# Optimization experiments

Hardware: AMD Instinct MI355X
Metric: run time of the kernel (lower is better)

Reference implementation:

```python
import jax, jax.numpy as jnp
import numpy as np

T_STEPS, N_GRID = 730, 8000
NEARZERO = 1e-5
# parameter bounds, order: tt ddf alpha beta stor retip fscn scx flz stot cgw resmax k1 k2 k3 k4 k5 k6
_BOUNDS = [(-3,5),(0,20),(0,1),(0,1),(0,5),(0,50),(0,1),(0,1),(0.005,0.995),(1,2000),(0,20),(1,300),(0,1),(1,5),(0,1),(0,1),(0,1),(0,1)]
_LO = jnp.array([b[0] for b in _BOUNDS], dtype=jnp.float32)
_HI = jnp.array([b[1] for b in _BOUNDS], dtype=jnp.float32)


def setup_inputs() -> dict:
    key = jax.random.key(0)
    kx, kp = jax.random.split(key)
    x = jax.random.uniform(kx, (T_STEPS, N_GRID, 3), dtype=jnp.float32)
    # scale forcings to physical ranges: prcp in [0,10) mm/d, tmean in [-2,6) C, pet in [0,5) mm/d
    x = x * jnp.array([10.0, 8.0, 5.0], dtype=jnp.float32) + jnp.array([0.0, -2.0, 0.0], dtype=jnp.float32)
    parameters = jax.random.normal(kp, (T_STEPS, N_GRID, 18), dtype=jnp.float32)
    return {"x": x, "parameters": parameters}


def _prms_forward(x, parameters):
    # static params: sigmoid of NN output at static_idx = warm_up - 1 = -1, scaled to bounds
    p = jax.nn.sigmoid(parameters[-1, :, :18])            # [N, 18]
    p = _LO + p * (_HI - _LO)
    p = p[:, :, None]                                      # [N, 18, 1]  (nmul = 1)
    (tt, ddf, alpha, beta, stor, retip, fscn, scx, flz, stot,
     cgw, resmax, k1, k2, k3, k4, k5, k6) = [p[:, i] for i in range(18)]
    scn = fscn * scx
    remx = (1.0 - flz) * stot
    smax = flz * stot

    Pm = x[:, :, 0:1]    # precipitation [T, N, 1]
    Tm = x[:, :, 1:2]    # mean temperature
    PETm = x[:, :, 2:3]  # potential ET

    n_grid = x.shape[1]
    s0 = jnp.full((n_grid, 1), 0.001, dtype=jnp.float32)
    init = (s0, s0, s0, s0, s0, s0, s0)  # snow, XIN, RSTOR, RECHR, SMAV, RES, GW

    def step(state, inp):
        snow, xin, rstor, rechr, smav, res, gw = state
        PRECIP, temp, Ep = inp
        # snow partition and melt (delta_t = 1)
        is_snow = (temp <= tt).astype(jnp.float32)
        flux_ps = PRECIP * is_snow
        flux_pr = PRECIP * (1.0 - is_snow)
        snow = snow + flux_ps
        flux_m = jnp.maximum(ddf * (temp - tt), 0.0)
        flux_m = jnp.minimum(flux_m, snow)
        snow = jnp.maximum(snow - flux_m, NEARZERO)
        # interception
        flux_pim = flux_pr * (1.0 - beta)
        flux_psm = flux_pr * beta
        flux_pby = flux_psm * (1.0 - alpha)
        flux_pin = flux_psm * alpha
        xin = xin + flux_pin
        flux_ptf = jnp.maximum(xin - stor, 0.0)
        xin = jnp.maximum(xin - flux_ptf, NEARZERO)
        flux_ein = jnp.minimum(Ep * beta, xin)
        xin = jnp.maximum(xin - flux_ein, NEARZERO)
        # impervious reservoir
        flux_mim = flux_m * (1.0 - beta)
        flux_msm = flux_m * beta
        rstor = rstor + flux_mim + flux_pim
        flux_sas = jnp.maximum(rstor - retip, 0.0)
        rstor = jnp.maximum(rstor - flux_sas, NEARZERO)
        flux_eim = jnp.minimum((1.0 - beta) * Ep, rstor)
        rstor = jnp.maximum(rstor - flux_eim, NEARZERO)
        # surface runoff / infiltration to recharge zone
        sro_lin = jnp.clip(scn + (scx - scn) * (rechr / remx), 0.0, 1.0)
        inflow = flux_msm + flux_ptf + flux_pby
        flux_sro = sro_lin * inflow
        flux_inf = inflow - flux_sro
        rechr = rechr + flux_inf
        flux_pc = jnp.maximum(rechr - remx, 0.0)
        rechr = rechr - flux_pc
        evap_max_a = jnp.maximum(rechr / remx * (Ep - flux_ein - flux_eim), 0.0)
        flux_ea = jnp.minimum(evap_max_a, rechr)
        rechr = jnp.maximum(rechr - flux_ea, NEARZERO)
        # lower soil moisture zone
        smav = smav + flux_pc
        flux_excs = jnp.maximum(smav - smax, 0.0)
        smav = smav - flux_excs
        transp = jnp.where(rechr < (Ep - flux_ein - flux_eim),
                           jnp.maximum(smav / smax * (Ep - flux_ein - flux_eim - flux_ea), 0.0),
                           jnp.zeros_like(smav))
        transp = jnp.minimum(transp, smav)
        smav = jnp.maximum(smav - transp, NEARZERO)
        # seepage and subsurface reservoir
        flux_sep = jnp.minimum(cgw, flux_excs)
        flux_qres = jnp.maximum(flux_excs - flux_sep, 0.0)
        res = res + flux_qres
        flux_gad = k1 * (res / resmax) ** k2
        flux_gad = jnp.minimum(flux_gad, res)
        res = jnp.maximum(res - flux_gad, NEARZERO)
        flux_ras = k3 * res + k4 * res * res
        flux_ras = jnp.minimum(flux_ras, res)
        res = jnp.maximum(res - flux_ras, NEARZERO)
        # groundwater
        gw = gw + flux_gad + flux_sep
        flux_bas = k5 * gw
        gw = jnp.maximum(gw - flux_bas, NEARZERO)
        flux_snk = k6 * gw
        gw = jnp.maximum(gw - flux_snk, NEARZERO)
        q = flux_sas + flux_sro + flux_bas + flux_ras
        return (snow, xin, rstor, rechr, smav, res, gw), q

    _, Q = jax.lax.scan(step, init, (Pm, Tm, PETm))
    return Q  # [T, N, 1]


def reference(x, parameters):
    return _prms_forward(x, parameters)
```

## Files before the change

### kernel.cpp

```cpp
#include <hip/hip_runtime.h>
#include <math.h>

#define T_STEPS 730
#define N_GRID  8000
#define NEARZERO 1e-5f

__constant__ float c_lo[18] = {-3.f, 0.f, 0.f, 0.f, 0.f, 0.f, 0.f, 0.f, 0.005f, 1.f,    0.f, 1.f,   0.f, 1.f, 0.f, 0.f, 0.f, 0.f};
__constant__ float c_hi[18] = { 5.f, 20.f, 1.f, 1.f, 5.f, 50.f, 1.f, 1.f, 0.995f, 2000.f, 20.f, 300.f, 1.f, 5.f, 1.f, 1.f, 1.f, 1.f};

#define EXP2F(v) __builtin_amdgcn_exp2f(v)
#define LOG2F(v) __builtin_amdgcn_logf(v)

constexpr int CH  = 10;
constexpr int NCH = T_STEPS / CH;

__global__ __launch_bounds__(256, 1) void prms_kernel(
    const float* __restrict__ x,
    const float* __restrict__ params,
    float* __restrict__ out)
{
    const int lane = threadIdx.x & 63;
    const int wv   = threadIdx.x >> 6;
    const int i    = blockIdx.x * 64 + lane;

    __shared__ float4 c0a[2][CH][64];
    __shared__ float4 c0b[2][CH][64];
    __shared__ float4 c1 [2][CH][64];
    __shared__ float2 c2 [2][CH][64];

    const float* pp = params + ((size_t)(T_STEPS - 1) * N_GRID + (size_t)i) * 18;
    float pr[18];
#pragma unroll
    for (int j = 0; j < 18; ++j) {
        float s = 1.0f / (1.0f + expf(-pp[j]));
        pr[j] = c_lo[j] + s * (c_hi[j] - c_lo[j]);
    }
    const float tt = pr[0],  ddf = pr[1], alpha = pr[2], beta = pr[3];
    const float stor = pr[4], retip = pr[5], fscn = pr[6], scx = pr[7];
    const float flz = pr[8],  stot = pr[9], cgw = pr[10], resmax = pr[11];
    const float k1 = pr[12],  k2 = pr[13], k3 = pr[14], k4 = pr[15];
    const float k5 = pr[16],  k6 = pr[17];

    const float ombeta   = 1.0f - beta;
    const float omalpha  = 1.0f - alpha;
    const float scn      = fscn * scx;
    const float remx     = (1.0f - flz) * stot;
    const float smax     = flz * stot;
    const float inv_remx = 1.0f / remx;
    const float inv_smax = 1.0f / smax;
    const float omscn    = 1.0f - scn;
    const float omk3     = 1.0f - k3;
    const float omk56    = (1.0f - k5) * (1.0f - k6);
    const float dscn     = (scx - scn) * inv_remx;
    const float pow_c2   = fmaf(k2, LOG2F(1.0f / resmax), LOG2F(k1));

    if (wv == 0) {
        float snow = 0.001f;
        float3 buf[CH];
#pragma unroll
        for (int u = 0; u < CH; ++u) {
            const float* q = x + ((size_t)u * N_GRID + (size_t)i) * 3;
            buf[u] = make_float3(q[0], q[1], q[2]);
        }

        for (int c = 0; c < NCH + 3; ++c) {
            if (c < NCH) {
                float3 nbuf[CH];
                const bool more = (c + 1 < NCH);
                if (more) {
#pragma unroll
                    for (int u = 0; u < CH; ++u) {
                        const float* q = x + ((size_t)((c + 1) * CH + u) * N_GRID + (size_t)i) * 3;
                        nbuf[u] = make_float3(q[0], q[1], q[2]);
                    }
                }

#pragma unroll
                for (int u = 0; u < CH; ++u) {
                    const float PRECIP = buf[u].x;
                    const float temp   = buf[u].y;
                    const float Ep     = buf[u].z;

                    const bool  snowy    = (temp <= tt);
                    const float flux_ps  = snowy ? PRECIP : 0.0f;
                    const float flux_pr  = PRECIP - flux_ps;
                    const float m0       = fmaxf(ddf * (temp - tt), 0.0f);
                    const float ps_m     = flux_ps - m0;

                    const float snow1  = snow + flux_ps;
                    const float flux_m = fminf(m0, snow1);
                    snow = fmaxf(snow + ps_m, NEARZERO);

                    const float flux_pim = flux_pr * ombeta;
                    const float flux_psm = flux_pr * beta;
                    const float flux_pby = flux_psm * omalpha;
                    const float flux_pin = flux_psm * alpha;
                    const float eb       = Ep * beta;
                    const float eim_cap  = ombeta * Ep;
                    const float flux_mim = flux_m * ombeta;
                    const float rin      = flux_mim + flux_pim;
                    const float msm      = flux_m * beta;

                    c0a[c & 1][u][lane] = make_float4(flux_pin, eb, rin, eim_cap);
                    c0b[c & 1][u][lane] = make_float4(msm, flux_pby, Ep, 0.0f);
                }

                if (more) {
#pragma unroll
                    for (int u = 0; u < CH; ++u) buf[u] = nbuf[u];
                }
            }
            __syncthreads();
        }
    } else if (wv == 1) {
        float xin = 0.001f, rstor = 0.001f;

        for (int c = 0; c < NCH + 3; ++c) {
            const int cc = c - 1;
            if (cc >= 0 && cc < NCH) {
#pragma unroll
                for (int u = 0; u < CH; ++u) {
                    const float4 a = c0a[cc & 1][u][lane];
                    const float4 b = c0b[cc & 1][u][lane];
                    const float flux_pin = a.x, eb = a.y, rin = a.z, eim_cap = a.w;
                    const float msm = b.x, pby = b.y, Ep = b.z;

                    const float pin_eb    = flux_pin - eb;
                    const float stor_eb   = stor - eb;
                    const float retip_eim = retip - eim_cap;

                    const float xin1     = xin + flux_pin;
                    const float flux_ptf = fmaxf(xin1 - stor, 0.0f);
                    const float xin2     = fmaxf(fminf(xin1, stor), NEARZERO);
                    const float flux_ein = fminf(eb, xin2);
                    xin = fmaxf(fminf(xin + pin_eb, stor_eb), NEARZERO);

                    const float rstor1   = rstor + rin;
                    const float flux_sas = fmaxf(rstor1 - retip, 0.0f);
                    const float rstor2   = fmaxf(fminf(rstor1, retip), NEARZERO);
                    const float flux_eim = fminf(eim_cap, rstor2);
                    rstor = fmaxf(fminf(rstor1 - eim_cap, retip_eim), NEARZERO);

                    const float inflow = msm + (flux_ptf + pby);
                    const float ep_rem = Ep - flux_ein - flux_eim;
                    c1[cc & 1][u][lane] = make_float4(inflow, ep_rem, flux_sas, 0.0f);
                }
            }
            __syncthreads();
        }
    } else if (wv == 2) {
        float rechr = 0.001f, smav = 0.001f;

        for (int c = 0; c < NCH + 3; ++c) {
            const int cc = c - 2;
            if (cc >= 0 && cc < NCH) {
#pragma unroll
                for (int u = 0; u < CH; ++u) {
                    const float4 h = c1[cc & 1][u][lane];
                    const float inflow = h.x, ep_rem = h.y, flux_sas = h.z;

                    const float tkeep    = fminf(fmaxf(fmaf(-dscn, rechr, omscn), 0.0f), 1.0f);
                    const float flux_inf = inflow * tkeep;
                    const float flux_sro = inflow - flux_inf;

                    const float rechr1  = fmaf(inflow, tkeep, rechr);
                    const float flux_pc = fmaxf(rechr1 - remx, 0.0f);
                    const float rechr2  = fminf(rechr1, remx);
                    const float cfac    = inv_remx * ep_rem;
                    const float emax    = rechr2 * cfac;
                    const float flux_ea = fminf(emax, rechr2);
                    rechr = fmaxf(rechr2 * (1.0f - cfac), NEARZERO);

                    const float smav1     = smav + flux_pc;
                    const float flux_excs = fmaxf(smav1 - smax, 0.0f);
                    const float smav2     = fminf(smav1, smax);
                    const float gfac      = inv_smax * (ep_rem - flux_ea);
                    const float hkeep     = (rechr < ep_rem) ? (1.0f - gfac) : 1.0f;
                    smav = fmaxf(smav2 * hkeep, NEARZERO);

                    const float s2 = flux_sas + flux_sro;
                    c2[cc & 1][u][lane] = make_float2(flux_excs, s2);
                }
            }
            __syncthreads();
        }
    } else {
        float res = 0.001f, gw = 0.001f;

        for (int c = 0; c < NCH + 3; ++c) {
            const int cc = c - 3;
            if (cc >= 0 && cc < NCH) {
#pragma unroll
                for (int u = 0; u < CH; ++u) {
                    const float2 h = c2[cc & 1][u][lane];
                    const float flux_excs = h.x, s2 = h.y;

                    const float flux_sep  = fminf(cgw, flux_excs);
                    const float flux_qres = fmaxf(flux_excs - cgw, 0.0f);
                    const float res1      = res + flux_qres;
                    const float gad0      = EXP2F(fmaf(k2, LOG2F(res1), pow_c2));
                    const float flux_gad  = fminf(gad0, res1);
                    const float res2      = fmaxf(res1 - gad0, NEARZERO);
                    const float ras0      = fmaf(k4, res2, k3) * res2;
                    const float flux_ras  = fminf(ras0, res2);
                    res = fmaxf(res2 * fmaf(-k4, res2, omk3), NEARZERO);

                    const float gw1      = gw + (flux_gad + flux_sep);
                    const float flux_bas = k5 * gw1;
                    gw = fmaxf(gw1 * omk56, NEARZERO);

                    const float q = s2 + (flux_bas + flux_ras);
                    out[(size_t)(cc * CH + u) * N_GRID + (size_t)i] = q;
                }
            }
            __syncthreads();
        }
    }
}

extern "C" void kernel_launch(void* const* d_in, const int* in_sizes, int n_in,
                              void* d_out, int out_size, void* d_ws, size_t ws_size,
                              hipStream_t stream) {
    const float* x      = (const float*)d_in[0];
    const float* params = (const float*)d_in[1];
    float* out          = (float*)d_out;
    prms_kernel<<<dim3(N_GRID / 64), dim3(256), 0, stream>>>(x, params, out);
}
```

Baseline: 597.7 us.

## Replace block barriers with per-wave LDS progress flags in stage pipeline

Each of the four waves in the block runs one stage of the recurrence. The per-chunk __syncthreads lockstep is replaced by producer/consumer progress counters in LDS, using workgroup-scope acquire/release atomics and spin-waits on a double buffer. Stages can now drift relative to each other, so a slow stage (for example the pow in the last wave, or the global loads in the first) no longer stalls every wave at each chunk. The cost is spin-polling LDS, which competes for issue slots. Correctness depends on the memory ordering between lane 0's store and the other lanes' buffer writes.

```diff
diff --git a/kernel.cpp b/kernel.cpp
--- a/kernel.cpp
+++ b/kernel.cpp
@@ -13,6 +13,13 @@
 
 constexpr int CH  = 10;
 constexpr int NCH = T_STEPS / CH;
+
+__device__ __forceinline__ int ld_acq(int* p) {
+    return __hip_atomic_load(p, __ATOMIC_ACQUIRE, __HIP_MEMORY_SCOPE_WORKGROUP);
+}
+__device__ __forceinline__ void st_rel(int* p, int v) {
+    __hip_atomic_store(p, v, __ATOMIC_RELEASE, __HIP_MEMORY_SCOPE_WORKGROUP);
+}
 
 __global__ __launch_bounds__(256, 1) void prms_kernel(
     const float* __restrict__ x,
@@ -27,6 +34,10 @@
     __shared__ float4 c0b[2][CH][64];
     __shared__ float4 c1 [2][CH][64];
     __shared__ float2 c2 [2][CH][64];
+    __shared__ int prog[4];
+
+    if (threadIdx.x < 4) prog[threadIdx.x] = 0;
+    __syncthreads();
 
     const float* pp = params + ((size_t)(T_STEPS - 1) * N_GRID + (size_t)i) * 18;
     float pr[18];
@@ -63,157 +74,160 @@
             buf[u] = make_float3(q[0], q[1], q[2]);
         }
 
-        for (int c = 0; c < NCH + 3; ++c) {
-            if (c < NCH) {
-                float3 nbuf[CH];
-                const bool more = (c + 1 < NCH);
-                if (more) {
-#pragma unroll
-                    for (int u = 0; u < CH; ++u) {
-                        const float* q = x + ((size_t)((c + 1) * CH + u) * N_GRID + (size_t)i) * 3;
-                        nbuf[u] = make_float3(q[0], q[1], q[2]);
-                    }
+        for (int c = 0; c < NCH; ++c) {
+            if (c >= 2) { while (ld_acq(&prog[1]) < c - 1) {} }
+
+            float3 nbuf[CH];
+            const bool more = (c + 1 < NCH);
+            if (more) {
+#pragma unroll
+                for (int u = 0; u < CH; ++u) {
+                    const float* q = x + ((size_t)((c + 1) * CH + u) * N_GRID + (size_t)i) * 3;
+                    nbuf[u] = make_float3(q[0], q[1], q[2]);
                 }
-
-#pragma unroll
-                for (int u = 0; u < CH; ++u) {
-                    const float PRECIP = buf[u].x;
-                    const float temp   = buf[u].y;
-                    const float Ep     = buf[u].z;
-
-                    const bool  snowy    = (temp <= tt);
-                    const float flux_ps  = snowy ? PRECIP : 0.0f;
-                    const float flux_pr  = PRECIP - flux_ps;
-                    const float m0       = fmaxf(ddf * (temp - tt), 0.0f);
-                    const float ps_m     = flux_ps - m0;
-
-                    const float snow1  = snow + flux_ps;
-                    const float flux_m = fminf(m0, snow1);
-                    snow = fmaxf(snow + ps_m, NEARZERO);
-
-                    const float flux_pim = flux_pr * ombeta;
-                    const float flux_psm = flux_pr * beta;
-                    const float flux_pby = flux_psm * omalpha;
-                    const float flux_pin = flux_psm * alpha;
-                    const float eb       = Ep * beta;
-                    const float eim_cap  = ombeta * Ep;
-                    const float flux_mim = flux_m * ombeta;
-                    const float rin      = flux_mim + flux_pim;
-                    const float msm      = flux_m * beta;
-
-                    c0a[c & 1][u][lane] = make_float4(flux_pin, eb, rin, eim_cap);
-                    c0b[c & 1][u][lane] = make_float4(msm, flux_pby, Ep, 0.0f);
-                }
-
-                if (more) {
-#pragma unroll
-                    for (int u = 0; u < CH; ++u) buf[u] = nbuf[u];
-                }
-            }
-            __syncthreads();
+            }
+
+#pragma unroll
+            for (int u = 0; u < CH; ++u) {
+                const float PRECIP = buf[u].x;
+                const float temp   = buf[u].y;
+                const float Ep     = buf[u].z;
+
+                const bool  snowy    = (temp <= tt);
+                const float flux_ps  = snowy ? PRECIP : 0.0f;
+                const float flux_pr  = PRECIP - flux_ps;
+                const float m0       = fmaxf(ddf * (temp - tt), 0.0f);
+                const float ps_m     = flux_ps - m0;
+
+                const float snow1  = snow + flux_ps;
+                const float flux_m = fminf(m0, snow1);
+                snow = fmaxf(snow + ps_m, NEARZERO);
+
+                const float flux_pim = flux_pr * ombeta;
+                const float flux_psm = flux_pr * beta;
+                const float flux_pby = flux_psm * omalpha;
+                const float flux_pin = flux_psm * alpha;
+                const float eb       = Ep * beta;
+                const float eim_cap  = ombeta * Ep;
+                const float flux_mim = flux_m * ombeta;
+                const float rin      = flux_mim + flux_pim;
+                const float msm      = flux_m * beta;
+
+                c0a[c & 1][u][lane] = make_float4(flux_pin, eb, rin, eim_cap);
+                c0b[c & 1][u][lane] = make_float4(msm, flux_pby, Ep, 0.0f);
+            }
+
+            if (lane == 0) st_rel(&prog[0], c + 1);
+
+            if (more) {
+#pragma unroll
+                for (int u = 0; u < CH; ++u) buf[u] = nbuf[u];
+            }
         }
     } else if (wv == 1) {
         float xin = 0.001f, rstor = 0.001f;
 
-        for (int c = 0; c < NCH + 3; ++c) {
-            const int cc = c - 1;
-            if (cc >= 0 && cc < NCH) {
-#pragma unroll
-                for (int u = 0; u < CH; ++u) {
-                    const float4 a = c0a[cc & 1][u][lane];
-                    const float4 b = c0b[cc & 1][u][lane];
-                    const float flux_pin = a.x, eb = a.y, rin = a.z, eim_cap = a.w;
-                    const float msm = b.x, pby = b.y, Ep = b.z;
-
-                    const float pin_eb    = flux_pin - eb;
-                    const float stor_eb   = stor - eb;
-                    const float retip_eim = retip - eim_cap;
-
-                    const float xin1     = xin + flux_pin;
-                    const float flux_ptf = fmaxf(xin1 - stor, 0.0f);
-                    const float xin2     = fmaxf(fminf(xin1, stor), NEARZERO);
-                    const float flux_ein = fminf(eb, xin2);
-                    xin = fmaxf(fminf(xin + pin_eb, stor_eb), NEARZERO);
-
-                    const float rstor1   = rstor + rin;
-                    const float flux_sas = fmaxf(rstor1 - retip, 0.0f);
-                    const float rstor2   = fmaxf(fminf(rstor1, retip), NEARZERO);
-                    const float flux_eim = fminf(eim_cap, rstor2);
-                    rstor = fmaxf(fminf(rstor1 - eim_cap, retip_eim), NEARZERO);
-
-                    const float inflow = msm + (flux_ptf + pby);
-                    const float ep_rem = Ep - flux_ein - flux_eim;
-                    c1[cc & 1][u][lane] = make_float4(inflow, ep_rem, flux_sas, 0.0f);
-                }
-            }
-            __syncthreads();
+        for (int c = 0; c < NCH; ++c) {
+            while (ld_acq(&prog[0]) < c + 1) {}
+            if (c >= 2) { while (ld_acq(&prog[2]) < c - 1) {} }
+
+#pragma unroll
+            for (int u = 0; u < CH; ++u) {
+                const float4 a = c0a[c & 1][u][lane];
+                const float4 b = c0b[c & 1][u][lane];
+                const float flux_pin = a.x, eb = a.y, rin = a.z, eim_cap = a.w;
+                const float msm = b.x, pby = b.y, Ep = b.z;
+
+                const float pin_eb    = flux_pin - eb;
+                const float stor_eb   = stor - eb;
+                const float retip_eim = retip - eim_cap;
+
+                const float xin1     = xin + flux_pin;
+                const float flux_ptf = fmaxf(xin1 - stor, 0.0f);
+                const float xin2     = fmaxf(fminf(xin1, stor), NEARZERO);
+                const float flux_ein = fminf(eb, xin2);
+                xin = fmaxf(fminf(xin + pin_eb, stor_eb), NEARZERO);
+
+                const float rstor1   = rstor + rin;
+                const float flux_sas = fmaxf(rstor1 - retip, 0.0f);
+                const float rstor2   = fmaxf(fminf(rstor1, retip), NEARZERO);
+                const float flux_eim = fminf(eim_cap, rstor2);
+                rstor = fmaxf(fminf(rstor1 - eim_cap, retip_eim), NEARZERO);
+
+                const float inflow = msm + (flux_ptf + pby);
+                const float ep_rem = Ep - flux_ein - flux_eim;
+                c1[c & 1][u][lane] = make_float4(inflow, ep_rem, flux_sas, 0.0f);
+            }
+
+            if (lane == 0) st_rel(&prog[1], c + 1);
         }
     } else if (wv == 2) {
         float rechr = 0.001f, smav = 0.001f;
 
-        for (int c = 0; c < NCH + 3; ++c) {
-            const int cc = c - 2;
-            if (cc >= 0 && cc < NCH) {
-#pragma unroll
-                for (int u = 0; u < CH; ++u) {
-                    const float4 h = c1[cc & 1][u][lane];
-                    const float inflow = h.x, ep_rem = h.y, flux_sas = h.z;
-
-                    const float tkeep    = fminf(fmaxf(fmaf(-dscn, rechr, omscn), 0.0f), 1.0f);
-                    const float flux_inf = inflow * tkeep;
-                    const float flux_sro = inflow - flux_inf;
-
-                    const float rechr1  = fmaf(inflow, tkeep, rechr);
-                    const float flux_pc = fmaxf(rechr1 - remx, 0.0f);
-                    const float rechr2  = fminf(rechr1, remx);
-                    const float cfac    = inv_remx * ep_rem;
-                    const float emax    = rechr2 * cfac;
-                    const float flux_ea = fminf(emax, rechr2);
-                    rechr = fmaxf(rechr2 * (1.0f - cfac), NEARZERO);
-
-                    const float smav1     = smav + flux_pc;
-                    const float flux_excs = fmaxf(smav1 - smax, 0.0f);
-                    const float smav2     = fminf(smav1, smax);
-                    const float gfac      = inv_smax * (ep_rem - flux_ea);
-                    const float hkeep     = (rechr < ep_rem) ? (1.0f - gfac) : 1.0f;
-                    smav = fmaxf(smav2 * hkeep, NEARZERO);
-
-                    const float s2 = flux_sas + flux_sro;
-                    c2[cc & 1][u][lane] = make_float2(flux_excs, s2);
-                }
-            }
-            __syncthreads();
+        for (int c = 0; c < NCH; ++c) {
+            while (ld_acq(&prog[1]) < c + 1) {}
+            if (c >= 2) { while (ld_acq(&prog[3]) < c - 1) {} }
+
+#pragma unroll
+            for (int u = 0; u < CH; ++u) {
+                const float4 h = c1[c & 1][u][lane];
+                const float inflow = h.x, ep_rem = h.y, flux_sas = h.z;
+
+                const float tkeep    = fminf(fmaxf(fmaf(-dscn, rechr, omscn), 0.0f), 1.0f);
+                const float flux_inf = inflow * tkeep;
+                const float flux_sro = inflow - flux_inf;
+
+                const float rechr1  = fmaf(inflow, tkeep, rechr);
+                const float flux_pc = fmaxf(rechr1 - remx, 0.0f);
+                const float rechr2  = fminf(rechr1, remx);
+                const float cfac    = inv_remx * ep_rem;
+                const float emax    = rechr2 * cfac;
+                const float flux_ea = fminf(emax, rechr2);
+                rechr = fmaxf(rechr2 * (1.0f - cfac), NEARZERO);
+
+                const float smav1     = smav + flux_pc;
+                const float flux_excs = fmaxf(smav1 - smax, 0.0f);
+                const float smav2     = fminf(smav1, smax);
+                const float gfac      = inv_smax * (ep_rem - flux_ea);
+                const float hkeep     = (rechr < ep_rem) ? (1.0f - gfac) : 1.0f;
+                smav = fmaxf(smav2 * hkeep, NEARZERO);
+
+                const float s2 = flux_sas + flux_sro;
+                c2[c & 1][u][lane] = make_float2(flux_excs, s2);
+            }
+
+            if (lane == 0) st_rel(&prog[2], c + 1);
         }
     } else {
         float res = 0.001f, gw = 0.001f;
 
-        for (int c = 0; c < NCH + 3; ++c) {
-            const int cc = c - 3;
-            if (cc >= 0 && cc < NCH) {
-#pragma unroll
-                for (int u = 0; u < CH; ++u) {
-                    const float2 h = c2[cc & 1][u][lane];
-                    const float flux_excs = h.x, s2 = h.y;
-
-                    const float flux_sep  = fminf(cgw, flux_excs);
-                    const float flux_qres = fmaxf(flux_excs - cgw, 0.0f);
-                    const float res1      = res + flux_qres;
-                    const float gad0      = EXP2F(fmaf(k2, LOG2F(res1), pow_c2));
-                    const float flux_gad  = fminf(gad0, res1);
-                    const float res2      = fmaxf(res1 - gad0, NEARZERO);
-                    const float ras0      = fmaf(k4, res2, k3) * res2;
-                    const float flux_ras  = fminf(ras0, res2);
-                    res = fmaxf(res2 * fmaf(-k4, res2, omk3), NEARZERO);
-
-                    const float gw1      = gw + (flux_gad + flux_sep);
-                    const float flux_bas = k5 * gw1;
-                    gw = fmaxf(gw1 * omk56, NEARZERO);
-
-                    const float q = s2 + (flux_bas + flux_ras);
-                    out[(size_t)(cc * CH + u) * N_GRID + (size_t)i] = q;
-                }
-            }
-            __syncthreads();
+        for (int c = 0; c < NCH; ++c) {
+            while (ld_acq(&prog[2]) < c + 1) {}
+
+#pragma unroll
+            for (int u = 0; u < CH; ++u) {
+                const float2 h = c2[c & 1][u][lane];
+                const float flux_excs = h.x, s2 = h.y;
+
+                const float flux_sep  = fminf(cgw, flux_excs);
+                const float flux_qres = fmaxf(flux_excs - cgw, 0.0f);
+                const float res1      = res + flux_qres;
+                const float gad0      = EXP2F(fmaf(k2, LOG2F(res1), pow_c2));
+                const float flux_gad  = fminf(gad0, res1);
+                const float res2      = fmaxf(res1 - gad0, NEARZERO);
+                const float ras0      = fmaf(k4, res2, k3) * res2;
+                const float flux_ras  = fminf(ras0, res2);
+                res = fmaxf(res2 * fmaf(-k4, res2, omk3), NEARZERO);
+
+                const float gw1      = gw + (flux_gad + flux_sep);
+                const float flux_bas = k5 * gw1;
+                gw = fmaxf(gw1 * omk56, NEARZERO);
+
+                const float q = s2 + (flux_bas + flux_ras);
+                out[(size_t)(c * CH + u) * N_GRID + (size_t)i] = q;
+            }
+
+            if (lane == 0) st_rel(&prog[3], c + 1);
         }
     }
 }
```

New measurement: 601.8 us. About the same (+0.7%).
